# Kernel tuning notes

Measured on AMD Instinct MI355X. Metric: run time of the kernel, lower is better.

## Reference

```python
import jax, jax.numpy as jnp
import numpy as np

DIM = 256
HEADS = 8
WS = 7                      # window size
N = WS * WS                 # tokens per window = 49
SCALE = (DIM // HEADS) ** -0.5
B_ = 4096                   # total windows (64 images * 64 windows)
NW = 64                     # windows per image (mask.shape[0])


def _rel_index():
    # Swin relative position index, computed exactly as in the torch module.
    coords = np.stack(np.meshgrid(np.arange(WS), np.arange(WS), indexing='ij'))  # [2,WS,WS]
    cf = coords.reshape(2, -1)                          # [2, N]
    rel = cf[:, :, None] - cf[:, None, :]               # [2, N, N]
    rel = rel.transpose(1, 2, 0).copy()                 # [N, N, 2]
    rel[:, :, 0] += WS - 1
    rel[:, :, 1] += WS - 1
    rel[:, :, 0] *= 2 * WS - 1
    return rel.sum(-1)                                  # [N, N] in [0, (2WS-1)^2)


def setup_inputs() -> dict:
    key = jax.random.key(0)
    ks = jax.random.split(key, 7)
    x = jax.random.normal(ks[0], (B_, N, DIM), dtype=jnp.float32)
    mask = jax.random.normal(ks[1], (NW, N, N), dtype=jnp.float32)
    qkv_w = jax.random.normal(ks[2], (3 * DIM, DIM), dtype=jnp.float32) * 0.02
    qkv_b = jax.random.normal(ks[3], (3 * DIM,), dtype=jnp.float32) * 0.02
    proj_w = jax.random.normal(ks[4], (DIM, DIM), dtype=jnp.float32) * 0.02
    proj_b = jax.random.normal(ks[5], (DIM,), dtype=jnp.float32) * 0.02
    bias_table = jax.random.normal(ks[6], ((2 * WS - 1) ** 2, HEADS), dtype=jnp.float32) * 0.02
    rel_idx = jnp.asarray(_rel_index(), dtype=jnp.int32)
    return {"x": x, "mask": mask, "qkv_w": qkv_w, "qkv_b": qkv_b,
            "proj_w": proj_w, "proj_b": proj_b, "bias_table": bias_table,
            "rel_idx": rel_idx}


def reference(x, mask, qkv_w, qkv_b, proj_w, proj_b, bias_table, rel_idx):
    Bw, n, C = x.shape
    hd = C // HEADS
    # fused qkv projection: [Bw, n, 3C] -> [3, Bw, H, n, hd]
    qkv = (x @ qkv_w.T + qkv_b).reshape(Bw, n, 3, HEADS, hd).transpose(2, 0, 3, 1, 4)
    q, k, v = qkv[0] * SCALE, qkv[1], qkv[2]
    attn = jnp.einsum('bhnd,bhmd->bhnm', q, k)                     # [Bw,H,n,n]
    # relative position bias gather: [n*n, H] -> [H, n, n]
    bias = bias_table[rel_idx.reshape(-1)].reshape(n, n, HEADS).transpose(2, 0, 1)
    attn = attn + bias[None]
    nW = mask.shape[0]
    # shift mask add: group windows per image
    attn = attn.reshape(Bw // nW, nW, HEADS, n, n) + mask[None, :, None]
    attn = jax.nn.softmax(attn.reshape(Bw, HEADS, n, n), axis=-1)
    out = jnp.einsum('bhnm,bhmd->bhnd', attn, v)                   # [Bw,H,n,hd]
    out = out.transpose(0, 2, 1, 3).reshape(Bw, n, C)
    return out @ proj_w.T + proj_b
```

## Files before the change

### kernel.cpp

```cpp
#include <hip/hip_runtime.h>
#include <hip/hip_bf16.h>

#define NTOK 49
#define DIM 256
#define HEADS 8
#define HD 32
#define SCALE 0.17677669529663687f

typedef float f32x4 __attribute__((ext_vector_type(4)));
typedef short bf16x8 __attribute__((ext_vector_type(8)));
typedef short bf16x4 __attribute__((ext_vector_type(4)));

__device__ __forceinline__ unsigned short f2bf(float f) {
    union { __hip_bfloat16 h; unsigned short u; } c;
    c.h = __float2bfloat16(f);
    return c.u;
}
__device__ __forceinline__ float bf2f(unsigned short u) {
    return __builtin_bit_cast(float, (unsigned)u << 16);
}
__device__ __forceinline__ uint2 pack4(float a, float b, float c, float d) {
    uint2 r;
    r.x = (unsigned)f2bf(a) | ((unsigned)f2bf(b) << 16);
    r.y = (unsigned)f2bf(c) | ((unsigned)f2bf(d) << 16);
    return r;
}

__device__ __forceinline__ f32x4 mfma16(uint2 a, uint2 b, f32x4 c) {
    bf16x4 av = __builtin_bit_cast(bf16x4, a);
    bf16x4 bv = __builtin_bit_cast(bf16x4, b);
#if __has_builtin(__builtin_amdgcn_mfma_f32_16x16x16bf16_1k)
    return __builtin_amdgcn_mfma_f32_16x16x16bf16_1k(av, bv, c, 0, 0, 0);
#elif __has_builtin(__builtin_amdgcn_mfma_f32_16x16x16_bf16)
    return __builtin_amdgcn_mfma_f32_16x16x16_bf16(av, bv, c, 0, 0, 0);
#else
    f32x4 d;
    asm volatile("v_mfma_f32_16x16x16_bf16 %0, %1, %2, %3"
                 : "=v"(d) : "v"(av), "v"(bv), "v"(c));
    return d;
#endif
}

__global__ void k0_prep(const float* __restrict__ qkv_w, const float* __restrict__ proj_w,
                        const float* __restrict__ mask, const float* __restrict__ bias_table,
                        const int* __restrict__ rel_idx,
                        unsigned short* __restrict__ wqf, unsigned short* __restrict__ wpf,
                        unsigned short* __restrict__ bmf, int total)
{
    int i = blockIdx.x * 256 + threadIdx.x;
    if (i >= total) return;
    if (i < 196608) {
        int j = i & 7, q = i >> 3;
        int lane = q & 63; q >>= 6;
        int ks2 = q & 7;  q >>= 3;
        int tt = q % 6;   q /= 6;
        int h  = q;
        int n96 = tt * 16 + (lane & 15);
        int seg = n96 >> 5, ch = n96 & 31;
        wqf[i] = f2bf(qkv_w[(seg * 256 + h * HD + ch) * 256 + ks2 * 32 + (lane >> 4) * 8 + j]);
    } else if (i < 262144) {
        int u = i - 196608;
        int j = u & 7, q = u >> 3;
        int lane = q & 63; q >>= 6;
        int ks2 = q & 7;  q >>= 3;
        int bt = q;
        int n = (bt >> 3) * 128 + (bt & 7) * 16 + (lane & 15);
        wpf[u] = f2bf(proj_w[n * 256 + ks2 * 32 + (lane >> 4) * 8 + j]);
    } else {
        int u = i - 262144;
        int j = u & 3;
        int lane = (u >> 2) & 63;
        int g = u >> 8;
        int mt = g & 3, ct = (g >> 2) & 3, h = (g >> 4) & 7, ws = g >> 7;
        int q = ct * 16 + (lane & 15);
        int key = mt * 16 + ((lane >> 4) & 3) * 4 + j;
        float v = 0.f;
        if (q < NTOK && key < NTOK)
            v = mask[ws * 2401 + q * NTOK + key] + bias_table[rel_idx[q * NTOK + key] * HEADS + h];
        bmf[u] = f2bf(v);
    }
}

__global__ __launch_bounds__(256, 2)
void k1_fused(
    const float* __restrict__ x,
    const float* __restrict__ qkv_b,
    const float* __restrict__ pb,
    const unsigned short* __restrict__ wqf,
    const unsigned short* __restrict__ wpf,
    const unsigned short* __restrict__ bmf,
    float* __restrict__ out)
{
    __shared__ unsigned short xs[49 * 256];

    const int t = threadIdx.x, bw = blockIdx.x;
    const int lane = t & 63, wv = t >> 6;
    const int l15 = lane & 15, l16 = lane >> 4;

    const float* xw = x + (size_t)bw * NTOK * DIM;
    for (int cidx = t; cidx < NTOK * 32; cidx += 256) {
        int row = cidx >> 5, c8 = cidx & 31;
        f32x4 a = __builtin_nontemporal_load((const f32x4*)(xw + row * DIM + c8 * 8));
        f32x4 b = __builtin_nontemporal_load((const f32x4*)(xw + row * DIM + c8 * 8 + 4));
        bf16x8 v;
        v[0] = (short)f2bf(a[0]); v[1] = (short)f2bf(a[1]);
        v[2] = (short)f2bf(a[2]); v[3] = (short)f2bf(a[3]);
        v[4] = (short)f2bf(b[0]); v[5] = (short)f2bf(b[1]);
        v[6] = (short)f2bf(b[2]); v[7] = (short)f2bf(b[3]);
        *(bf16x8*)(xs + row * 256 + ((c8 * 8) ^ ((row & 7) << 3))) = v;
    }
    __syncthreads();

    int arow[4];
    #pragma unroll
    for (int i4 = 0; i4 < 4; ++i4) {
        int r = i4 * 16 + l15;
        arow[i4] = r > 48 ? 48 : r;
    }

    uint2 ob[2][2][4];

    #pragma unroll
    for (int hh = 0; hh < 2; ++hh) {
        const int h = wv + 4 * hh;
        const unsigned short* wb = wqf + (size_t)h * 24576;
        uint2 qpk[4][2], kpk[4][2], vpk[4][2];
        uint2 bmu[4][4];

        #pragma unroll
        for (int p = 0; p < 2; ++p) {
            f32x4 aq[4], ak[4], av[4];
            #pragma unroll
            for (int nt = 0; nt < 4; ++nt) {
                aq[nt] = (f32x4){0.f,0.f,0.f,0.f};
                ak[nt] = (f32x4){0.f,0.f,0.f,0.f};
                av[nt] = (f32x4){0.f,0.f,0.f,0.f};
            }
            __builtin_amdgcn_s_setprio(1);
            #pragma unroll
            for (int ks2 = 0; ks2 < 8; ++ks2) {
                bf16x8 xf[4];
                #pragma unroll
                for (int nt = 0; nt < 4; ++nt)
                    xf[nt] = *(const bf16x8*)(xs + arow[nt] * 256 +
                               ((ks2 * 32 + l16 * 8) ^ ((arow[nt] & 7) << 3)));
                bf16x8 wqf_ = *(const bf16x8*)(wb + ((p    ) * 8 + ks2) * 512 + lane * 8);
                bf16x8 wkf_ = *(const bf16x8*)(wb + ((2 + p) * 8 + ks2) * 512 + lane * 8);
                bf16x8 wvf_ = *(const bf16x8*)(wb + ((4 + p) * 8 + ks2) * 512 + lane * 8);
                #pragma unroll
                for (int nt = 0; nt < 4; ++nt) {
                    aq[nt] = __builtin_amdgcn_mfma_f32_16x16x32_bf16(wqf_, xf[nt], aq[nt], 0, 0, 0);
                    ak[nt] = __builtin_amdgcn_mfma_f32_16x16x32_bf16(wkf_, xf[nt], ak[nt], 0, 0, 0);
                    av[nt] = __builtin_amdgcn_mfma_f32_16x16x32_bf16(xf[nt], wvf_, av[nt], 0, 0, 0);
                }
            }
            __builtin_amdgcn_s_setprio(0);

            if (p == 1) {
                #pragma unroll
                for (int ct = 0; ct < 4; ++ct)
                    #pragma unroll
                    for (int mt = 0; mt < 4; ++mt)
                        bmu[ct][mt] = *(const uint2*)(bmf +
                            (((size_t)(((bw & 63) * 8 + h) * 16 + ct * 4 + mt)) << 8) + (lane << 2));
            }

            float4 bq4 = *(const float4*)(qkv_b + h * HD + p * 16 + l16 * 4);
            float4 bk4 = *(const float4*)(qkv_b + 256 + h * HD + p * 16 + l16 * 4);
            float  bvs = qkv_b[512 + h * HD + p * 16 + l15];
            #pragma unroll
            for (int nt = 0; nt < 4; ++nt) {
                qpk[nt][p] = pack4((aq[nt][0] + bq4.x) * SCALE, (aq[nt][1] + bq4.y) * SCALE,
                                   (aq[nt][2] + bq4.z) * SCALE, (aq[nt][3] + bq4.w) * SCALE);
                kpk[nt][p] = pack4(ak[nt][0] + bk4.x, ak[nt][1] + bk4.y,
                                   ak[nt][2] + bk4.z, ak[nt][3] + bk4.w);
                vpk[nt][p] = pack4(av[nt][0] + bvs, av[nt][1] + bvs,
                                   av[nt][2] + bvs, av[nt][3] + bvs);
            }
        }

        #pragma unroll
        for (int ct = 0; ct < 4; ++ct) {
            f32x4 sT[4];
            __builtin_amdgcn_s_setprio(1);
            #pragma unroll
            for (int mt = 0; mt < 4; ++mt) {
                f32x4 z = (f32x4){0.f,0.f,0.f,0.f};
                sT[mt] = mfma16(kpk[mt][1], qpk[ct][1],
                                mfma16(kpk[mt][0], qpk[ct][0], z));
            }
            __builtin_amdgcn_s_setprio(0);

            float vv[4][4];
            float mx = -1e30f;
            #pragma unroll
            for (int mt = 0; mt < 4; ++mt) {
                float b0 = bf2f((unsigned short)(bmu[ct][mt].x & 0xffff));
                float b1 = bf2f((unsigned short)(bmu[ct][mt].x >> 16));
                float b2 = bf2f((unsigned short)(bmu[ct][mt].y & 0xffff));
                float b3 = bf2f((unsigned short)(bmu[ct][mt].y >> 16));
                float bj[4] = {b0, b1, b2, b3};
                #pragma unroll
                for (int j = 0; j < 4; ++j) {
                    float v = sT[mt][j] + bj[j];
                    if (mt * 16 + l16 * 4 + j >= NTOK) v = -1e30f;
                    vv[mt][j] = v;
                    mx = fmaxf(mx, v);
                }
            }
            mx = fmaxf(mx, __shfl_xor(mx, 16));
            mx = fmaxf(mx, __shfl_xor(mx, 32));
            float sum = 0.f;
            #pragma unroll
            for (int mt = 0; mt < 4; ++mt)
                #pragma unroll
                for (int j = 0; j < 4; ++j) {
                    float e = __expf(vv[mt][j] - mx);
                    vv[mt][j] = e;
                    sum += e;
                }
            sum += __shfl_xor(sum, 16);
            sum += __shfl_xor(sum, 32);
            float inv = 1.f / sum;

            uint2 ppk[4];
            #pragma unroll
            for (int mt = 0; mt < 4; ++mt)
                ppk[mt] = pack4(vv[mt][0] * inv, vv[mt][1] * inv,
                                vv[mt][2] * inv, vv[mt][3] * inv);

            f32x4 o0 = (f32x4){0.f,0.f,0.f,0.f};
            f32x4 o1 = (f32x4){0.f,0.f,0.f,0.f};
            __builtin_amdgcn_s_setprio(1);
            #pragma unroll
            for (int mt = 0; mt < 4; ++mt) {
                o0 = mfma16(vpk[mt][0], ppk[mt], o0);
                o1 = mfma16(vpk[mt][1], ppk[mt], o1);
            }
            __builtin_amdgcn_s_setprio(0);
            ob[hh][0][ct] = pack4(o0[0], o0[1], o0[2], o0[3]);
            ob[hh][1][ct] = pack4(o1[0], o1[1], o1[2], o1[3]);
        }
    }

    __syncthreads();

    #pragma unroll
    for (int hh = 0; hh < 2; ++hh) {
        #pragma unroll
        for (int a = 0; a < 2; ++a) {
            #pragma unroll
            for (int ct = 0; ct < 4; ++ct) {
                int tok = ct * 16 + l15;
                if (tok < NTOK) {
                    int ch0 = (wv + 4 * hh) * HD + a * 16 + l16 * 4;
                    int ad = tok * 256 + ((ch0 & ~7) ^ ((tok & 7) << 3)) + (ch0 & 7);
                    *(uint2*)(xs + ad) = ob[hh][a][ct];
                }
            }
        }
    }
    __syncthreads();

    f32x4 pacc[4][4];
    #pragma unroll
    for (int ct = 0; ct < 4; ++ct)
        #pragma unroll
        for (int u = 0; u < 4; ++u) pacc[ct][u] = (f32x4){0.f,0.f,0.f,0.f};

    __builtin_amdgcn_s_setprio(1);
    #pragma unroll
    for (int ks2 = 0; ks2 < 8; ++ks2) {
        bf16x8 xf[4];
        #pragma unroll
        for (int ct = 0; ct < 4; ++ct)
            xf[ct] = *(const bf16x8*)(xs + arow[ct] * 256 +
                       ((ks2 * 32 + l16 * 8) ^ ((arow[ct] & 7) << 3)));
        #pragma unroll
        for (int u = 0; u < 4; ++u) {
            bf16x8 wf = *(const bf16x8*)(wpf + (size_t)((wv * 4 + u) * 8 + ks2) * 512 + lane * 8);
            #pragma unroll
            for (int ct = 0; ct < 4; ++ct)
                pacc[ct][u] = __builtin_amdgcn_mfma_f32_16x16x32_bf16(wf, xf[ct], pacc[ct][u], 0, 0, 0);
        }
    }
    __builtin_amdgcn_s_setprio(0);

    #pragma unroll
    for (int u = 0; u < 4; ++u) {
        int bt = wv * 4 + u;
        int base = (bt >> 3) * 128 + (bt & 7) * 16;
        float4 pb4 = *(const float4*)(pb + base + l16 * 4);
        #pragma unroll
        for (int ct = 0; ct < 4; ++ct) {
            int tok = ct * 16 + l15;
            if (tok < NTOK) {
                f32x4 r;
                r[0] = pacc[ct][u][0] + pb4.x;
                r[1] = pacc[ct][u][1] + pb4.y;
                r[2] = pacc[ct][u][2] + pb4.z;
                r[3] = pacc[ct][u][3] + pb4.w;
                __builtin_nontemporal_store(r,
                    (f32x4*)(out + ((size_t)bw * NTOK + tok) * DIM + base + l16 * 4));
            }
        }
    }
}

extern "C" void kernel_launch(void* const* d_in, const int* in_sizes, int n_in,
                              void* d_out, int out_size, void* d_ws, size_t ws_size,
                              hipStream_t stream) {
    const float* x    = (const float*)d_in[0];
    const float* mask = (const float*)d_in[1];
    const float* qkvw = (const float*)d_in[2];
    const float* qkvb = (const float*)d_in[3];
    const float* pw   = (const float*)d_in[4];
    const float* pb   = (const float*)d_in[5];
    const float* bt   = (const float*)d_in[6];
    const int*   ri   = (const int*)d_in[7];
    float* out = (float*)d_out;

    unsigned short* wqf = (unsigned short*)d_ws;
    unsigned short* wpf = wqf + 196608;
    unsigned short* bmf = (unsigned short*)((char*)d_ws + 524288);

    const int nwin = in_sizes[0] / (NTOK * DIM);
    const int total = 262144 + 64 * HEADS * 16 * 256;

    k0_prep<<<(total + 255) / 256, 256, 0, stream>>>(qkvw, pw, mask, bt, ri,
                                                     wqf, wpf, bmf, total);
    k1_fused<<<nwin, 256, 0, stream>>>(x, qkvb, pb, wqf, wpf, bmf, out);
}
```

Before: 238.2 us.

## Cut register pressure with separate LDS attention buffer and per-tile mask loads

```diff
diff --git a/kernel.cpp b/kernel.cpp
--- a/kernel.cpp
+++ b/kernel.cpp
@@ -81,7 +81,7 @@
     }
 }
 
-__global__ __launch_bounds__(256, 2)
+__global__ __launch_bounds__(256, 3)
 void k1_fused(
     const float* __restrict__ x,
     const float* __restrict__ qkv_b,
@@ -92,6 +92,7 @@
     float* __restrict__ out)
 {
     __shared__ unsigned short xs[49 * 256];
+    __shared__ unsigned short aos[49 * 256];
 
     const int t = threadIdx.x, bw = blockIdx.x;
     const int lane = t & 63, wv = t >> 6;
@@ -118,14 +119,11 @@
         arow[i4] = r > 48 ? 48 : r;
     }
 
-    uint2 ob[2][2][4];
-
     #pragma unroll
     for (int hh = 0; hh < 2; ++hh) {
         const int h = wv + 4 * hh;
         const unsigned short* wb = wqf + (size_t)h * 24576;
         uint2 qpk[4][2], kpk[4][2], vpk[4][2];
-        uint2 bmu[4][4];
 
         #pragma unroll
         for (int p = 0; p < 2; ++p) {
@@ -156,15 +154,6 @@
             }
             __builtin_amdgcn_s_setprio(0);
 
-            if (p == 1) {
-                #pragma unroll
-                for (int ct = 0; ct < 4; ++ct)
-                    #pragma unroll
-                    for (int mt = 0; mt < 4; ++mt)
-                        bmu[ct][mt] = *(const uint2*)(bmf +
-                            (((size_t)(((bw & 63) * 8 + h) * 16 + ct * 4 + mt)) << 8) + (lane << 2));
-            }
-
             float4 bq4 = *(const float4*)(qkv_b + h * HD + p * 16 + l16 * 4);
             float4 bk4 = *(const float4*)(qkv_b + 256 + h * HD + p * 16 + l16 * 4);
             float  bvs = qkv_b[512 + h * HD + p * 16 + l15];
@@ -181,6 +170,12 @@
 
         #pragma unroll
         for (int ct = 0; ct < 4; ++ct) {
+            uint2 bmu4[4];
+            #pragma unroll
+            for (int mt = 0; mt < 4; ++mt)
+                bmu4[mt] = *(const uint2*)(bmf +
+                    (((size_t)(((bw & 63) * 8 + h) * 16 + ct * 4 + mt)) << 8) + (lane << 2));
+
             f32x4 sT[4];
             __builtin_amdgcn_s_setprio(1);
             #pragma unroll
@@ -195,11 +190,10 @@
             float mx = -1e30f;
             #pragma unroll
             for (int mt = 0; mt < 4; ++mt) {
-                float b0 = bf2f((unsigned short)(bmu[ct][mt].x & 0xffff));
-                float b1 = bf2f((unsigned short)(bmu[ct][mt].x >> 16));
-                float b2 = bf2f((unsigned short)(bmu[ct][mt].y & 0xffff));
-                float b3 = bf2f((unsigned short)(bmu[ct][mt].y >> 16));
-                float bj[4] = {b0, b1, b2, b3};
+                float bj[4] = { bf2f((unsigned short)(bmu4[mt].x & 0xffff)),
+                                bf2f((unsigned short)(bmu4[mt].x >> 16)),
+                                bf2f((unsigned short)(bmu4[mt].y & 0xffff)),
+                                bf2f((unsigned short)(bmu4[mt].y >> 16)) };
                 #pragma unroll
                 for (int j = 0; j < 4; ++j) {
                     float v = sT[mt][j] + bj[j];
@@ -238,28 +232,19 @@
                 o1 = mfma16(vpk[mt][1], ppk[mt], o1);
             }
             __builtin_amdgcn_s_setprio(0);
-            ob[hh][0][ct] = pack4(o0[0], o0[1], o0[2], o0[3]);
-            ob[hh][1][ct] = pack4(o1[0], o1[1], o1[2], o1[3]);
+
+            int tok = ct * 16 + l15;
+            if (tok < NTOK) {
+                int ch0 = h * HD + l16 * 4;
+                int ad0 = tok * 256 + ((ch0 & ~7) ^ ((tok & 7) << 3)) + (ch0 & 7);
+                *(uint2*)(aos + ad0) = pack4(o0[0], o0[1], o0[2], o0[3]);
+                int ch1 = h * HD + 16 + l16 * 4;
+                int ad1 = tok * 256 + ((ch1 & ~7) ^ ((tok & 7) << 3)) + (ch1 & 7);
+                *(uint2*)(aos + ad1) = pack4(o1[0], o1[1], o1[2], o1[3]);
+            }
         }
     }
 
-    __syncthreads();
-
-    #pragma unroll
-    for (int hh = 0; hh < 2; ++hh) {
-        #pragma unroll
-        for (int a = 0; a < 2; ++a) {
-            #pragma unroll
-            for (int ct = 0; ct < 4; ++ct) {
-                int tok = ct * 16 + l15;
-                if (tok < NTOK) {
-                    int ch0 = (wv + 4 * hh) * HD + a * 16 + l16 * 4;
-                    int ad = tok * 256 + ((ch0 & ~7) ^ ((tok & 7) << 3)) + (ch0 & 7);
-                    *(uint2*)(xs + ad) = ob[hh][a][ct];
-                }
-            }
-        }
-    }
     __syncthreads();
 
     f32x4 pacc[4][4];
@@ -274,7 +259,7 @@
         bf16x8 xf[4];
         #pragma unroll
         for (int ct = 0; ct < 4; ++ct)
-            xf[ct] = *(const bf16x8*)(xs + arow[ct] * 256 +
+            xf[ct] = *(const bf16x8*)(aos + arow[ct] * 256 +
                        ((ks2 * 32 + l16 * 8) ^ ((arow[ct] & 7) << 3)));
         #pragma unroll
         for (int u = 0; u < 4; ++u) {
```

After: 224.4 us. 5.8% less time.
